# Kernel optimization log

Hardware: AMD Instinct MI355X
Metric: run time of the kernel (lower is better)

Reference implementation:

```python
import jax, jax.numpy as jnp
import numpy as np
from jax import lax

LOG2PI = 1.8378770664093453


def _lstm_last(x, Wih, Whh, b, reverse):
    # x: [N, T, D]; returns hidden output at the LAST timestep index (torch output[:, -1])
    N = x.shape[0]
    H = Whh.shape[1]
    xg = jnp.einsum('ntd,gd->tng', x, Wih) + b  # [T, N, 4H], gate order i,f,g,o

    def step(carry, g_in):
        h, c = carry
        g = g_in + h @ Whh.T
        i, f, gg, o = jnp.split(g, 4, axis=-1)
        c = jax.nn.sigmoid(f) * c + jax.nn.sigmoid(i) * jnp.tanh(gg)
        h = jax.nn.sigmoid(o) * jnp.tanh(c)
        return (h, c), h

    init = (jnp.zeros((N, H), x.dtype), jnp.zeros((N, H), x.dtype))
    _, hs = lax.scan(step, init, xg, reverse=reverse)
    return hs[-1]  # fw: full pass; bw(reverse=True): processed only last element, as torch


def _dvbf(x, u, eps1, eps, fw_Wih, fw_Whh, fw_b, bw_Wih, bw_Whh, bw_b,
          i1_w, i1_b, i2_w, i2_b, z1_w, z1_b, z2_w, z2_b,
          wp_w1, wp_b1, wp_w2, wp_b2, vp_w1, vp_b1, vp_w2, vp_b2,
          ob_w1, ob_b1, ob_w2, ob_b2, A, B, C):
    N, T, dx = x.shape
    dw = eps1.shape[1]
    # initial samples from bidirectional LSTM output at t = T-1 (fw || bw)
    h0 = jnp.concatenate([_lstm_last(x, fw_Wih, fw_Whh, fw_b, False),
                          _lstm_last(x, bw_Wih, bw_Whh, bw_b, True)], axis=1)
    p0 = jax.nn.relu(h0 @ i1_w.T + i1_b) @ i2_w.T + i2_b
    m0, s0_raw = jnp.split(p0, 2, axis=1)
    s0 = jnp.exp(s0_raw) + 1e-5
    w1 = m0 + s0 * eps1  # reparameterized torch.normal(mean, std)
    z1 = jax.nn.relu(w1 @ z1_w.T + z1_b) @ z2_w.T + z2_b

    def step(z_t, inp):
        x_t, u_t, e_t = inp
        pw = jnp.tanh(jnp.concatenate([x_t, z_t, u_t], axis=1) @ wp_w1.T + wp_b1) @ wp_w2.T + wp_b2
        m, s_raw = jnp.split(pw, 2, axis=1)
        s = jnp.exp(s_raw) + 0.01
        w_t = m + s * e_t
        alpha = jax.nn.softmax(
            jax.nn.relu(jnp.concatenate([z_t, u_t], axis=1) @ vp_w1.T + vp_b1) @ vp_w2.T + vp_b2,
            axis=1)
        z_n = (jnp.einsum('nm,mij,nj->ni', alpha, A, z_t)
               + jnp.einsum('nm,mij,nj->ni', alpha, B, u_t)
               + jnp.einsum('nm,mij,nj->ni', alpha, C, w_t))
        return z_n, (z_n, m, s)

    xs = (jnp.swapaxes(x[:, 1:], 0, 1), jnp.swapaxes(u[:, :T - 1], 0, 1), jnp.swapaxes(eps[:, 1:], 0, 1))
    _, (zs, ms, ss) = lax.scan(step, z1, xs)
    z = jnp.concatenate([z1[:, None], jnp.swapaxes(zs, 0, 1)], axis=1)        # [N,T,dz]
    w_mean = jnp.concatenate([m0[:, None], jnp.swapaxes(ms, 0, 1)], axis=1)   # [N,T,dw]
    w_std = jnp.concatenate([s0[:, None], jnp.swapaxes(ss, 0, 1)], axis=1)

    x_rec = jax.nn.relu(z @ ob_w1.T + ob_b1) @ ob_w2.T + ob_b2                # [N,T,dx]
    logprob_x = -0.5 * jnp.sum((x - x_rec) ** 2) - 0.5 * N * T * dx * LOG2PI
    # KL(N(m, diag(std)) || N(0, I)) -- the module uses std as the covariance diagonal
    kl = 0.5 * (jnp.sum(w_std) + jnp.sum(w_mean ** 2) - N * T * dw - jnp.sum(jnp.log(w_std)))
    return -(logprob_x - kl)


def setup_inputs() -> dict:
    key = jax.random.key(0)
    ks = iter(jax.random.split(key, 64))

    def rn(shape, s=1.0):
        return s * jax.random.normal(next(ks), shape, dtype=jnp.float32)

    N, T, DX, DU, DZ, DW, M, H = 512, 128, 256, 32, 128, 64, 16, 128
    S = 0.05  # weight scale keeps the recurrence stable
    return {
        'x': rn((N, T, DX)), 'u': rn((N, T, DU)),
        'eps1': rn((N, DW)), 'eps': rn((N, T, DW)),
        'fw_Wih': rn((4 * H, DX), S), 'fw_Whh': rn((4 * H, H), S), 'fw_b': rn((4 * H,), S),
        'bw_Wih': rn((4 * H, DX), S), 'bw_Whh': rn((4 * H, H), S), 'bw_b': rn((4 * H,), S),
        'i1_w': rn((H, 2 * H), S), 'i1_b': rn((H,), S), 'i2_w': rn((2 * DW, H), S), 'i2_b': rn((2 * DW,), S),
        'z1_w': rn((H, DW), S), 'z1_b': rn((H,), S), 'z2_w': rn((DZ, H), S), 'z2_b': rn((DZ,), S),
        'wp_w1': rn((H, DZ + DU + DX), S), 'wp_b1': rn((H,), S), 'wp_w2': rn((2 * DW, H), S), 'wp_b2': rn((2 * DW,), S),
        'vp_w1': rn((H, DZ + DU), S), 'vp_b1': rn((H,), S), 'vp_w2': rn((M, H), S), 'vp_b2': rn((M,), S),
        'ob_w1': rn((H, DZ), S), 'ob_b1': rn((H,), S), 'ob_w2': rn((DX, H), S), 'ob_b2': rn((DX,), S),
        'A': rn((M, DZ, DZ), S), 'B': rn((M, DZ, DU), S), 'C': rn((M, DZ, DW), S),
    }


def reference(x, u, eps1, eps, fw_Wih, fw_Whh, fw_b, bw_Wih, bw_Whh, bw_b,
              i1_w, i1_b, i2_w, i2_b, z1_w, z1_b, z2_w, z2_b,
              wp_w1, wp_b1, wp_w2, wp_b2, vp_w1, vp_b1, vp_w2, vp_b2,
              ob_w1, ob_b1, ob_w2, ob_b2, A, B, C):
    return _dvbf(x, u, eps1, eps, fw_Wih, fw_Whh, fw_b, bw_Wih, bw_Whh, bw_b,
                 i1_w, i1_b, i2_w, i2_b, z1_w, z1_b, z2_w, z2_b,
                 wp_w1, wp_b1, wp_w2, wp_b2, vp_w1, vp_b1, vp_w2, vp_b2,
                 ob_w1, ob_b1, ob_w2, ob_b2, A, B, C)
```

## Files before the change

### kernel.cpp

```cpp
#include <hip/hip_runtime.h>
#include <stdint.h>
#include <math.h>

#define NB  512
#define TT  128
#define DXX 256
#define DUU 32
#define DZZ 128
#define DWW 64
#define MMM 16
#define HHH 128
#define G4  512

typedef __attribute__((ext_vector_type(8))) short bf16x8;
typedef __attribute__((ext_vector_type(4))) float f32x4;
#define MFMA(a,b,c) __builtin_amdgcn_mfma_f32_16x16x32_bf16(a,b,c,0,0,0)
#define MF8(a,b,c)  __builtin_amdgcn_mfma_f32_16x16x32_fp8_fp8(a,b,c,0,0,0)

__device__ __forceinline__ float sigf(float x){ return 1.f/(1.f+__expf(-x)); }
__device__ __forceinline__ float fast_tanh(float x){
    float e = __expf(2.f*x);
    return 1.f - 2.f/(e + 1.f);
}
__device__ __forceinline__ unsigned int f2bf(float f){
    uint32_t u = __float_as_uint(f);
    uint32_t r = (u + 0x7fffu + ((u >> 16) & 1u)) >> 16;
    return r;
}
__device__ __forceinline__ float bf2f(unsigned short u){
    return __uint_as_float(((uint32_t)u) << 16);
}
__device__ __forceinline__ unsigned int f2e4m3(float f){
    uint32_t u = __float_as_uint(f);
    uint32_t s = (u >> 24) & 0x80u;
    uint32_t a = u & 0x7fffffffu;
    if (a >= 0x43e00000u) return s | 0x7eu;
    int exp = (int)(a >> 23) - 127;
    uint32_t mant = a & 0x7fffffu;
    uint32_t code;
    if (exp >= -6){
        uint32_t keep = ((uint32_t)(exp + 7) << 3) | (mant >> 20);
        uint32_t rem = mant & 0xfffffu;
        if (rem > 0x80000u || (rem == 0x80000u && (keep & 1))) keep++;
        code = keep;
        if (code >= 0x7fu) code = 0x7eu;
    } else {
        int rs = 14 - exp;
        if (rs >= 33) return s;
        uint64_t full = (uint64_t)(mant | 0x800000u);
        uint64_t q = full >> rs;
        uint64_t rem = full & (((uint64_t)1 << rs) - 1);
        uint64_t half = (uint64_t)1 << (rs - 1);
        if (rem > half || (rem == half && (q & 1))) q++;
        code = (uint32_t)q;
    }
    return s | code;
}

__device__ __forceinline__ void stage1k(const void* gsrc, void* ldst, int ln)
{
    __builtin_amdgcn_global_load_lds(
        (const __attribute__((address_space(1))) void*)((const char*)gsrc + ln*16),
        (__attribute__((address_space(3))) void*)ldst, 16, 0, 0);
}
__device__ __forceinline__ void stage32k(const void* gsrc, void* ldst, int tid)
{
    const char* g = (const char*)gsrc;
    char* l = (char*)ldst;
    const int lane = tid & 63;
    const int wv   = tid >> 6;
    #pragma unroll
    for (int it = 0; it < 8; it++){
        const int off = it*4096 + wv*1024;
        __builtin_amdgcn_global_load_lds(
            (const __attribute__((address_space(1))) void*)(g + off + lane*16),
            (__attribute__((address_space(3))) void*)(l + off),
            16, 0, 0);
    }
}

__global__ __launch_bounds__(256) void k_prep8b(
    const float* __restrict__ wp_w1, const float* __restrict__ wp_w2,
    const float* __restrict__ vp_w1, const float* __restrict__ vp_w2,
    const float* __restrict__ Amat,  const float* __restrict__ Bmat,
    const float* __restrict__ Cmat,  unsigned char* __restrict__ frag8)
{
    const int wv = blockIdx.x >> 3, c = blockIdx.x & 7;
    unsigned char* dst = frag8 + (size_t)(wv*8 + c)*8192;
    for (int d = threadIdx.x*4; d < 8192; d += 1024){
        uint32_t pk = 0;
        #pragma unroll
        for (int i = 0; i < 4; i++){
            const int B = d + i;
            const int f = 16*c + (B >> 9), r = B & 511;
            const int lane = r >> 3, jj = r & 7;
            const int col = wv*16 + (lane & 15);
            const int kk = (lane >> 4)*8 + jj;
            float v = 0.f;
            if (f < 4)       v = wp_w1[(size_t)col*416 + 256 + f*32 + kk];
            else if (f < 8)  v = vp_w1[(size_t)col*160 + (f-4)*32 + kk];
            else if (f < 12) v = wp_w2[(size_t)col*128 + (f-8)*32 + kk];
            else if (f < 16){ if (wv == 0) v = vp_w2[(size_t)(col&15)*128 + (f-12)*32 + kk]; }
            else {
                const int fi = f-16, m = fi/7, kt = fi%7;
                const int k = kt*32 + kk;
                if (k < 128)      v = Amat[((size_t)m*128 + col)*128 + k];
                else if (k < 160) v = Bmat[((size_t)m*128 + col)*32 + (k-128)];
                else              v = Cmat[((size_t)m*128 + col)*64 + (k-160)];
            }
            pk |= f2e4m3(v * 16.f) << (8*i);
        }
        *(uint32_t*)(dst + d) = pk;
    }
}

__global__ __launch_bounds__(256) void k_prep_p(
    const float* __restrict__ wp_w1, const float* __restrict__ vp_w1,
    unsigned short* __restrict__ fragP)
{
    const int ct = blockIdx.x / 10, f = blockIdx.x % 10;
    unsigned short* dst = fragP + (size_t)blockIdx.x*512;
    for (int e = threadIdx.x; e < 512; e += 256){
        const int lane = e >> 3, j = e & 7;
        const int col = 16*ct + (lane & 15);
        const int kk = (lane >> 4)*8 + j;
        float v;
        if (f < 8)      v = wp_w1[(size_t)col*416 + f*32 + kk];
        else if (f == 8) v = wp_w1[(size_t)col*416 + 384 + kk];
        else             v = vp_w1[(size_t)col*160 + 128 + kk];
        dst[e] = (unsigned short)f2bf(v);
    }
}

__global__ __launch_bounds__(256) void k_prep_xg(const float* __restrict__ Wih,
                                                 unsigned short* __restrict__ fragx)
{
    const int T = blockIdx.x;
    const int ct = T >> 3, kt = T & 7;
    unsigned short* dst = fragx + (size_t)T*512;
    for (int e = threadIdx.x; e < 512; e += 256){
        const int lane = e >> 3, j = e & 7;
        const int m16 = lane & 15, kq = lane >> 4;
        const int kk = 8*kq + j;
        float v = Wih[(size_t)(16*ct + m16)*DXX + 32*kt + kk];
        dst[e] = (unsigned short)f2bf(v);
    }
}

__global__ __launch_bounds__(256) void k_prep_lo(
    const float* __restrict__ Whh,
    const float* __restrict__ ob_w1, const float* __restrict__ ob_w2,
    unsigned short* __restrict__ blstm, unsigned short* __restrict__ bob)
{
    const int tile = blockIdx.x;
    unsigned short* dst; int lt;
    if (tile < 4){ dst = blstm + (size_t)tile*16384; lt = 1; }
    else { dst = bob + (size_t)(tile-4)*16384; lt = 2; }
    for (int e = threadIdx.x; e < 16384; e += 256){
        const int g = e >> 7, p = e & 127;
        const int s = p >> 3, j = p & 7;
        const int k = ((s ^ (g & 7)) << 3) | j;
        float v;
        if (lt == 1) v = Whh[(size_t)(tile*128 + g)*128 + k];
        else {
            const int tt = tile - 4;
            if (tt == 0) v = ob_w1[g*128 + k];
            else         v = ob_w2[(size_t)((tt-1)*128 + g)*128 + k];
        }
        dst[e] = (unsigned short)f2bf(v);
    }
}

__global__ __launch_bounds__(256) void k_prep_in(
    const float* __restrict__ U, const float* __restrict__ EPS,
    unsigned short* __restrict__ IE, unsigned char* __restrict__ IUf)
{
    const int b  = blockIdx.x;
    const int tt = blockIdx.y;
    const int n0 = b*16;
    unsigned short* de = IE + ((size_t)b*127 + tt)*1024;
    for (int h = threadIdx.x; h < 1024; h += 256){
        const int e2 = h >> 9, l = (h >> 3) & 63, j = h & 7;
        const int r = 8*e2 + (l >> 3);
        de[h] = (unsigned short)f2bf(EPS[((size_t)(n0+r)*TT + tt+1)*DWW + (l&7)*8 + j]);
    }
    unsigned char* df = IUf + ((size_t)b*127 + tt)*512;
    for (int h = threadIdx.x; h < 512; h += 256){
        const int smp = h >> 5, sp = (h >> 3) & 3, j = h & 7;
        const int ud = ((sp ^ (smp & 3))*8) + j;
        df[h] = (unsigned char)f2e4m3(U[((size_t)(n0+smp)*TT + tt)*DUU + ud]);
    }
}

__global__ __launch_bounds__(512) void k_pxu(
    const float* __restrict__ X, const float* __restrict__ U,
    const float* __restrict__ wp_b1, const float* __restrict__ vp_b1,
    const unsigned short* __restrict__ fragP,
    unsigned short* __restrict__ IPx, unsigned short* __restrict__ IPL)
{
    __shared__ __align__(16) short sXl[16*256];
    __shared__ __align__(16) short sUl[16*32];
    const int tid = threadIdx.x;
    const int b = blockIdx.x, t = blockIdx.y;
    const int n0 = b*16;
    const int wv = tid >> 6, ln = tid & 63;
    const int rr = ln & 15, q = ln >> 4;
    const int sx7 = rr & 7;
    {
        const int r = tid >> 5, sl = tid & 31;
        const float* xp = &X[((size_t)(n0+r)*TT + t+1)*DXX + sl*8];
        float4 a0 = *(const float4*)xp;
        float4 a1 = *(const float4*)(xp+4);
        int4 pk;
        pk.x = f2bf(a0.x) | (f2bf(a0.y)<<16);
        pk.y = f2bf(a0.z) | (f2bf(a0.w)<<16);
        pk.z = f2bf(a1.x) | (f2bf(a1.y)<<16);
        pk.w = f2bf(a1.z) | (f2bf(a1.w)<<16);
        *(int4*)&sXl[r*256 + ((sl ^ (r&7))<<3)] = pk;
    }
    {
        const int r = tid >> 5, cc = tid & 31;
        sUl[r*32 + (((cc>>3) ^ (r&3))<<3) + (cc&7)] =
            (unsigned short)f2bf(U[((size_t)(n0+r)*TT + t)*DUU + cc]);
    }
    __syncthreads();
    const short* pA = (const short*)fragP + (size_t)wv*10*512 + ln*8;
    f32x4 d = {0.f,0.f,0.f,0.f};
    #pragma unroll
    for (int kt = 0; kt < 8; kt++){
        bf16x8 a = *(const bf16x8*)(pA + kt*512);
        bf16x8 bx = *(const bf16x8*)&sXl[rr*256 + (((4*kt+q) ^ sx7)<<3)];
        d = MFMA(a, bx, d);
    }
    bf16x8 bu = *(const bf16x8*)&sUl[rr*32 + ((q ^ (rr&3))<<3)];
    d = MFMA(*(const bf16x8*)(pA + 8*512), bu, d);
    f32x4 dl = {0.f,0.f,0.f,0.f};
    dl = MFMA(*(const bf16x8*)(pA + 9*512), bu, dl);
    const f32x4 b1v = *(const f32x4*)&wp_b1[wv*16 + q*4];
    const f32x4 bLv = *(const f32x4*)&vp_b1[wv*16 + q*4];
    d = d + b1v;
    dl = dl + bLv;
    const size_t base = ((size_t)b*127 + t)*2048
                      + rr*128 + (((2*wv + (q>>1)) ^ sx7)<<3) + (q&1)*4;
    uint2 p1, p2;
    p1.x = f2bf(d[0]) | (f2bf(d[1])<<16);
    p1.y = f2bf(d[2]) | (f2bf(d[3])<<16);
    p2.x = f2bf(dl[0]) | (f2bf(dl[1])<<16);
    p2.y = f2bf(dl[2]) | (f2bf(dl[3])<<16);
    *(uint2*)&IPx[base] = p1;
    *(uint2*)&IPL[base] = p2;
}

template<int ACT>
__device__ void dense(const float* __restrict__ W, const float* __restrict__ bias,
                      int C, int K, const float* sIn, int ldi,
                      float* sOut, int ldo, float* sWt)
{
    const int tid = threadIdx.x;
    const int g   = tid & 127;
    const int rq  = tid >> 7;
    const int r0  = 2*rq, r1 = 2*rq+1;
    for (int cb = 0; cb < C; cb += 128){
        float acc0 = 0.f, acc1 = 0.f;
        for (int kb = 0; kb < K; kb += 64){
            const int kw = (K - kb < 64) ? (K - kb) : 64;
            __syncthreads();
            if (kw == 64){
                for (int l = tid; l < 128*64; l += 256){
                    int gg = l >> 6, kk = l & 63;
                    int cx = cb + gg;
                    sWt[gg*65 + kk] = (cx < C) ? W[(size_t)cx*K + kb + kk] : 0.f;
                }
            } else {
                for (int l = tid; l < 128*32; l += 256){
                    int gg = l >> 5, kk = l & 31;
                    int cx = cb + gg;
                    sWt[gg*65 + kk] = (cx < C) ? W[(size_t)cx*K + kb + kk] : 0.f;
                }
            }
            __syncthreads();
            const float* ip0 = sIn + r0*ldi + kb;
            const float* ip1 = sIn + r1*ldi + kb;
            const float* wp  = sWt + g*65;
            #pragma unroll 8
            for (int k = 0; k < kw; k++){
                float wv = wp[k];
                acc0 += ip0[k]*wv;
                acc1 += ip1[k]*wv;
            }
        }
        int cx = cb + g;
        if (cx < C){
            float b = bias ? bias[cx] : 0.f;
            float v0 = acc0 + b, v1 = acc1 + b;
            if (ACT == 1){ v0 = fmaxf(v0, 0.f); v1 = fmaxf(v1, 0.f); }
            else if (ACT == 2){ v0 = fast_tanh(v0); v1 = fast_tanh(v1); }
            sOut[r0*ldo + cx] = v0;
            sOut[r1*ldo + cx] = v1;
        }
    }
}

__global__ __launch_bounds__(512) void k_xg2(const float* __restrict__ X,
                                             const unsigned short* __restrict__ fragx,
                                             const float* __restrict__ bias,
                                             unsigned short* __restrict__ xgb)
{
    __shared__ __align__(16) short sXl[16*256];
    const int tid = threadIdx.x;
    const size_t row0 = (size_t)blockIdx.x * 16;
    const int wv = tid >> 6, ln = tid & 63;
    const int rr = ln & 15, q = ln >> 4;
    const int sx7 = rr & 7;
    {
        const int r = tid >> 5, sl = tid & 31;
        const float* xp = &X[(row0 + r)*DXX + sl*8];
        float4 a0 = *(const float4*)xp;
        float4 a1 = *(const float4*)(xp+4);
        int4 pk;
        pk.x = f2bf(a0.x) | (f2bf(a0.y)<<16);
        pk.y = f2bf(a0.z) | (f2bf(a0.w)<<16);
        pk.z = f2bf(a1.x) | (f2bf(a1.y)<<16);
        pk.w = f2bf(a1.z) | (f2bf(a1.w)<<16);
        *(int4*)&sXl[r*256 + ((sl ^ (r&7))<<3)] = pk;
    }
    __syncthreads();
    #pragma unroll
    for (int ci = 0; ci < 4; ci++){
        const int ct = wv*4 + ci;
        const short* pA = (const short*)fragx + (size_t)(ct*8)*512 + ln*8;
        bf16x8 af[8];
        #pragma unroll
        for (int kt = 0; kt < 8; kt++) af[kt] = *(const bf16x8*)(pA + kt*512);
        f32x4 d = {0.f,0.f,0.f,0.f};
        #pragma unroll
        for (int kt = 0; kt < 8; kt++){
            bf16x8 b = *(const bf16x8*)&sXl[rr*256 + (((4*kt+q) ^ sx7)<<3)];
            d = MFMA(af[kt], b, d);
        }
        const f32x4 bb = *(const f32x4*)&bias[ct*16 + q*4];
        uint2 pk;
        pk.x = f2bf(d[0]+bb[0]) | (f2bf(d[1]+bb[1])<<16);
        pk.y = f2bf(d[2]+bb[2]) | (f2bf(d[3]+bb[3])<<16);
        *(uint2*)&xgb[(row0 + rr)*G4 + ct*16 + q*4] = pk;
    }
}

__global__ __launch_bounds__(256) void k_lstm(const unsigned short* __restrict__ xgb,
                                              const unsigned short* __restrict__ blob,
                                              float* __restrict__ h0)
{
    __shared__ __align__(16) char sWh[4][32768];
    __shared__ __align__(16) float sHh[2][128];
    const int tid = threadIdx.x;
    const int n0 = blockIdx.x * 2;
    const int g = tid & 127, rh = tid >> 7;
    #pragma unroll
    for (int i = 0; i < 4; i++)
        stage32k((const char*)blob + (size_t)i*32768, sWh[i], tid);
    sHh[tid >> 7][tid & 127] = 0.f;
    float cc = 0.f;
    asm volatile("s_waitcnt vmcnt(0)" ::: "memory");
    __syncthreads();
    const size_t xbase = ((size_t)(n0+rh)*TT)*G4 + g;
    for (int t = 0; t < TT; t++){
        float xv[4];
        #pragma unroll
        for (int ct = 0; ct < 4; ct++) xv[ct] = bf2f(xgb[xbase + (size_t)t*G4 + ct*128]);
        float a[4] = {0.f,0.f,0.f,0.f};
        #pragma unroll
        for (int s = 0; s < 16; s++){
            const float* ip = &sHh[rh][s*8];
            float4 u0 = *(const float4*)ip;
            float4 u1 = *(const float4*)(ip+4);
            float in[8] = {u0.x,u0.y,u0.z,u0.w,u1.x,u1.y,u1.z,u1.w};
            #pragma unroll
            for (int ct = 0; ct < 4; ct++){
                const uint32_t* wp = (const uint32_t*)(sWh[ct] + g*256 + ((s ^ (g & 7)) << 4));
                #pragma unroll
                for (int d = 0; d < 4; d++){
                    uint32_t w2 = wp[d];
                    a[ct] = fmaf(__uint_as_float(w2 << 16),        in[2*d],   a[ct]);
                    a[ct] = fmaf(__uint_as_float(w2 & 0xffff0000u), in[2*d+1], a[ct]);
                }
            }
        }
        __syncthreads();
        float ii = sigf(a[0] + xv[0]);
        float ff = sigf(a[1] + xv[1]);
        float gg = fast_tanh(a[2] + xv[2]);
        float oo = sigf(a[3] + xv[3]);
        cc = ff*cc + ii*gg;
        float hh = oo*fast_tanh(cc);
        sHh[rh][g] = hh;
        __syncthreads();
    }
    h0[(size_t)(n0+rh)*HHH + g] = sHh[rh][g];
}

__global__ __launch_bounds__(256) void k_init(
    const float* __restrict__ X,
    const float* __restrict__ bw_Wih, const float* __restrict__ bw_b,
    const float* __restrict__ i1w, const float* __restrict__ i1b,
    const float* __restrict__ i2w, const float* __restrict__ i2b,
    const float* __restrict__ z1w, const float* __restrict__ z1b,
    const float* __restrict__ z2w, const float* __restrict__ z2b,
    const float* __restrict__ eps1, const float* __restrict__ h0,
    float* __restrict__ zb, float* __restrict__ wm, float* __restrict__ wsd)
{
    __shared__ float sX[4*260];
    __shared__ float sG[4*516];
    __shared__ float sH0[4*260];
    __shared__ float sT[4*132];
    __shared__ float sP[4*132];
    __shared__ float sWt[128*65];
    const int tid = threadIdx.x;
    const int n0  = blockIdx.x * 4;
    for (int l = tid; l < 4*256; l += 256){
        int r = l >> 8, k = l & 255;
        sX[r*260+k] = X[((size_t)(n0+r)*TT + (TT-1))*DXX + k];
    }
    for (int l = tid; l < 4*128; l += 256){
        int r = l >> 7, j = l & 127;
        sH0[r*260+j] = h0[(size_t)(n0+r)*HHH + j];
    }
    dense<0>(bw_Wih, bw_b, 512, 256, sX, 260, sG, 516, sWt);
    __syncthreads();
    for (int l = tid; l < 4*128; l += 256){
        int r = l >> 7, j = l & 127;
        float gi = sG[r*516 + j];
        float gv = sG[r*516 + 256 + j];
        float go = sG[r*516 + 384 + j];
        float c  = sigf(gi)*fast_tanh(gv);
        sH0[r*260 + 128 + j] = sigf(go)*fast_tanh(c);
    }
    dense<1>(i1w, i1b, 128, 256, sH0, 260, sT, 132, sWt);
    dense<0>(i2w, i2b, 128, 128, sT, 132, sP, 132, sWt);
    __syncthreads();
    for (int l = tid; l < 4*64; l += 256){
        int r = l >> 6, j = l & 63;
        float m0 = sP[r*132 + j];
        float s0 = __expf(sP[r*132 + 64 + j]) + 1e-5f;
        float w1 = m0 + s0*eps1[(size_t)(n0+r)*DWW + j];
        wm[((size_t)(n0+r)*TT)*DWW + j]  = m0;
        wsd[((size_t)(n0+r)*TT)*DWW + j] = s0;
        sX[r*68 + j] = w1;
    }
    dense<1>(z1w, z1b, 128, 64, sX, 68, sT, 132, sWt);
    dense<0>(z2w, z2b, 128, 128, sT, 132, sP, 132, sWt);
    __syncthreads();
    for (int l = tid; l < 4*128; l += 256){
        int r = l >> 7, j = l & 127;
        zb[((size_t)(n0+r)*TT)*DZZ + j] = sP[r*132+j];
    }
}

#define VWAIT4() do{ asm volatile("s_waitcnt vmcnt(4)" ::: "memory"); \
                    __builtin_amdgcn_sched_barrier(0); }while(0)
#define LWAIT() do{ asm volatile("s_waitcnt lgkmcnt(0)" ::: "memory"); \
                    __builtin_amdgcn_sched_barrier(0); }while(0)
#define BAR()   __builtin_amdgcn_s_barrier()

__global__ __launch_bounds__(512) void k_scan(
    const float* __restrict__ wp_b2, const float* __restrict__ vp_b2,
    const unsigned char* __restrict__ frag8,
    const unsigned short* __restrict__ IPx, const unsigned short* __restrict__ IPL,
    const unsigned short* __restrict__ IE, const unsigned char* __restrict__ IUf,
    float* __restrict__ zb, float* __restrict__ wm, float* __restrict__ wsd)
{
    __shared__ __align__(16) short sRing[32768];
    __shared__ __align__(16) short sHead[32768];
    __shared__ __align__(16) short sPx[2048];
    __shared__ __align__(16) short sPL[2048];
    __shared__ __align__(16) char  sZf[2048];
    __shared__ __align__(16) char  sUf[2][512];
    __shared__ __align__(16) char  sWf[1024];
    __shared__ __align__(16) short sEr[1024];
    __shared__ __align__(16) char  sH1f[2048];
    __shared__ __align__(16) char  sH2f[2048];
    __shared__ __align__(16) float sPW[16*132];
    __shared__ __align__(16) float sL [16*20];
    __shared__ float sAl[16*17];

    const int tid = threadIdx.x;
    const int n0  = blockIdx.x * 16;
    const int wv  = tid >> 6;
    const int ln  = tid & 63;
    const int smp = ln & 15, q = ln >> 4;
    const int sx7 = smp & 7;
    char* ringB = (char*)sRing + wv*8192;
    char* headB = (char*)sHead + wv*8192;
    const unsigned char* myblob = frag8 + (size_t)wv*65536;

    const f32x4 bw2 = *(const f32x4*)&wp_b2[wv*16 + q*4];
    f32x4 bv2 = {0.f,0.f,0.f,0.f};
    if (wv == 0) bv2 = *(const f32x4*)&vp_b2[q*4];

    #define ISSUE_CHUNK(cc_) do{ const int c2_ = (cc_) % 14; \
        _Pragma("unroll") \
        for (int k4 = 0; k4 < 4; k4++) \
            stage1k(myblob + 8192 + (size_t)c2_*4096 + k4*1024, \
                    ringB + (c2_&1)*4096 + k4*1024, ln); }while(0)
    #define HF8(f_)    (*(const long*)(headB + (f_)*512 + ln*8))
    #define AF8(c_,p_) (*(const long*)(ringB + ((c_)&1)*4096 + (p_)*512 + ln*8))
    #define BH1F(t_) (*(const long*)&sH1f[smp*128 + (((4*(t_)+q) ^ sx7)<<3)])
    #define BH2F(t_) (*(const long*)&sH2f[smp*128 + (((4*(t_)+q) ^ sx7)<<3)])

    auto issue_inputs = [&](int tt){
        const size_t ib = (size_t)blockIdx.x*127 + tt;
        if (wv < 4) stage1k((const char*)IPx + ib*4096 + wv*1024, (char*)sPx + wv*1024, ln);
        else        stage1k((const char*)IPL + ib*4096 + (wv-4)*1024, (char*)sPL + (wv-4)*1024, ln);
        if (wv == 0)      stage1k((const char*)IE + ib*2048,        (char*)sEr,        ln);
        else if (wv == 1) stage1k((const char*)IE + ib*2048 + 1024, (char*)sEr + 1024, ln);
        else if (wv == 2){ if (ln < 32) stage1k((const char*)IUf + ib*512, sUf[tt&1], ln); }
    };

    issue_inputs(0);
    if (tid < 256){
        const int zs = tid >> 4, sl = tid & 15;
        const float* zp = &zb[((size_t)(n0+zs)*TT)*DZZ + sl*8];
        float4 a0 = *(const float4*)zp;
        float4 a1 = *(const float4*)(zp+4);
        uint2 p8;
        p8.x = f2e4m3(a0.x) | (f2e4m3(a0.y)<<8) | (f2e4m3(a0.z)<<16) | (f2e4m3(a0.w)<<24);
        p8.y = f2e4m3(a1.x) | (f2e4m3(a1.y)<<8) | (f2e4m3(a1.z)<<16) | (f2e4m3(a1.w)<<24);
        *(uint2*)&sZf[zs*128 + ((sl ^ (zs&7))<<3)] = p8;
    }
    #pragma unroll
    for (int k8 = 0; k8 < 8; k8++)
        stage1k(myblob + k8*1024, headB + k8*1024, ln);
    ISSUE_CHUNK(0);
    ISSUE_CHUNK(1);
    asm volatile("s_waitcnt vmcnt(0)" ::: "memory");
    __builtin_amdgcn_sched_barrier(0);
    LWAIT(); BAR();

    for (int t = 0; t < TT-1; t++){
        long bz0 = *(const long*)&sZf[smp*128 + (((0*4+q) ^ sx7)<<3)];
        long bz1 = *(const long*)&sZf[smp*128 + (((1*4+q) ^ sx7)<<3)];
        long bz2 = *(const long*)&sZf[smp*128 + (((2*4+q) ^ sx7)<<3)];
        long bz3 = *(const long*)&sZf[smp*128 + (((3*4+q) ^ sx7)<<3)];

        f32x4 d1a = {0.f,0.f,0.f,0.f}, d1b = {0.f,0.f,0.f,0.f};
        d1a = MF8(HF8(0), bz0, d1a); d1b = MF8(HF8(1), bz1, d1b);
        d1a = MF8(HF8(2), bz2, d1a); d1b = MF8(HF8(3), bz3, d1b);
        f32x4 d3a = {0.f,0.f,0.f,0.f}, d3b = {0.f,0.f,0.f,0.f};
        d3a = MF8(HF8(4), bz0, d3a); d3b = MF8(HF8(5), bz1, d3b);
        d3a = MF8(HF8(6), bz2, d3a); d3b = MF8(HF8(7), bz3, d3b);
        {
            const int basep = smp*128 + (((2*wv + (q>>1)) ^ sx7)<<3) + (q&1)*4;
            uint2 pxw = *(const uint2*)&sPx[basep];
            uint2 plw = *(const uint2*)&sPL[basep];
            f32x4 d1 = d1a + d1b, d3 = d3a + d3b;
            float v0 = fast_tanh(d1[0]*0.0625f + bf2f((unsigned short)(pxw.x & 0xffff)));
            float v1 = fast_tanh(d1[1]*0.0625f + bf2f((unsigned short)(pxw.x >> 16)));
            float v2 = fast_tanh(d1[2]*0.0625f + bf2f((unsigned short)(pxw.y & 0xffff)));
            float v3 = fast_tanh(d1[3]*0.0625f + bf2f((unsigned short)(pxw.y >> 16)));
            const int baseh = smp*128 + (((2*wv + (q>>1)) ^ sx7)<<3) + (q&1)*4;
            *(unsigned int*)&sH1f[baseh] =
                f2e4m3(v0) | (f2e4m3(v1)<<8) | (f2e4m3(v2)<<16) | (f2e4m3(v3)<<24);
            float w0 = fmaxf(d3[0]*0.0625f + bf2f((unsigned short)(plw.x & 0xffff)), 0.f);
            float w1 = fmaxf(d3[1]*0.0625f + bf2f((unsigned short)(plw.x >> 16)), 0.f);
            float w2 = fmaxf(d3[2]*0.0625f + bf2f((unsigned short)(plw.y & 0xffff)), 0.f);
            float w3 = fmaxf(d3[3]*0.0625f + bf2f((unsigned short)(plw.y >> 16)), 0.f);
            *(unsigned int*)&sH2f[baseh] =
                f2e4m3(w0) | (f2e4m3(w1)<<8) | (f2e4m3(w2)<<16) | (f2e4m3(w3)<<24);
        }
        LWAIT(); BAR();

        {
            f32x4 d2a = {0.f,0.f,0.f,0.f}, d2b = {0.f,0.f,0.f,0.f};
            d2a = MF8(HF8(8),  BH1F(0), d2a); d2b = MF8(HF8(9),  BH1F(1), d2b);
            d2a = MF8(HF8(10), BH1F(2), d2a); d2b = MF8(HF8(11), BH1F(3), d2b);
            f32x4 o = (d2a + d2b)*0.0625f + bw2;
            *(f32x4*)&sPW[smp*132 + wv*16 + q*4] = o;
            if (wv == 0){
                f32x4 d4a = {0.f,0.f,0.f,0.f}, d4b = {0.f,0.f,0.f,0.f};
                d4a = MF8(HF8(12), BH2F(0), d4a); d4b = MF8(HF8(13), BH2F(1), d4b);
                d4a = MF8(HF8(14), BH2F(2), d4a); d4b = MF8(HF8(15), BH2F(3), d4b);
                f32x4 o4 = (d4a + d4b)*0.0625f + bv2;
                *(f32x4*)&sL[smp*20 + q*4] = o4;
            }
        }
        LWAIT(); BAR();

        {
            const int cs = wv, cj = ln;
            float e0 = bf2f((unsigned short)sEr[cs*64 + cj]);
            float e1 = bf2f((unsigned short)sEr[(cs+8)*64 + cj]);
            float m0 = sPW[cs*132 + cj];
            float s0 = __expf(sPW[cs*132 + 64 + cj]) + 0.01f;
            float m1 = sPW[(cs+8)*132 + cj];
            float s1 = __expf(sPW[(cs+8)*132 + 64 + cj]) + 0.01f;
            float w0 = m0 + s0*e0;
            float w1 = m1 + s1*e1;
            wm [((size_t)(n0+cs  )*TT + t+1)*DWW + cj] = m0;
            wsd[((size_t)(n0+cs  )*TT + t+1)*DWW + cj] = s0;
            wm [((size_t)(n0+cs+8)*TT + t+1)*DWW + cj] = m1;
            wsd[((size_t)(n0+cs+8)*TT + t+1)*DWW + cj] = s1;
            const int sw = cj >> 3;
            sWf[ cs   *64 + ((sw ^ ( cs   &7))<<3) + (cj&7)] = (char)f2e4m3(w0);
            sWf[(cs+8)*64 + ((sw ^ ((cs+8)&7))<<3) + (cj&7)] = (char)f2e4m3(w1);
        }
        if (tid < 16){
            float mx = -1e30f;
            #pragma unroll
            for (int m = 0; m < 16; m++) mx = fmaxf(mx, sL[tid*20+m]);
            float ss = 0.f;
            float ex[16];
            #pragma unroll
            for (int m = 0; m < 16; m++){ ex[m] = __expf(sL[tid*20+m]-mx); ss += ex[m]; }
            float inv = 0.0625f/ss;
            #pragma unroll
            for (int m = 0; m < 16; m++) sAl[tid*17+m] = ex[m]*inv;
        }
        if (t < TT-2) issue_inputs(t+1);
        LWAIT(); BAR();

        long bu8 = *(const long*)&sUf[t&1][smp*32 + ((q ^ (smp&3))<<3)];
        long bw80 = *(const long*)&sWf[smp*64 + ((q ^ sx7)<<3)];
        long bw81 = *(const long*)&sWf[smp*64 + (((4+q) ^ sx7)<<3)];
        f32x4 zac = {0.f,0.f,0.f,0.f};
        f32x4 da = {0.f,0.f,0.f,0.f}, db = {0.f,0.f,0.f,0.f};
        #pragma unroll
        for (int c = 0; c < 14; c++){
            VWAIT4();
            #pragma unroll
            for (int p = 0; p < 8; p++){
                const int fi = 8*c + p;
                const int m  = fi/7, kt = fi%7;
                long a = AF8(c, p);
                long b;
                if (kt == 0) b = bz0;
                else if (kt == 1) b = bz1;
                else if (kt == 2) b = bz2;
                else if (kt == 3) b = bz3;
                else if (kt == 4) b = bu8;
                else if (kt == 5) b = bw80;
                else b = bw81;
                if (kt & 1) db = MF8(a, b, db);
                else        da = MF8(a, b, da);
                if (kt == 6){
                    const float al = sAl[smp*17 + m];
                    f32x4 s = da + db;
                    zac[0] += al*s[0]; zac[1] += al*s[1];
                    zac[2] += al*s[2]; zac[3] += al*s[3];
                    da = (f32x4){0.f,0.f,0.f,0.f};
                    db = (f32x4){0.f,0.f,0.f,0.f};
                }
            }
            ISSUE_CHUNK(c+2);
        }
        LWAIT(); BAR();

        {
            const int slotz = 2*wv + (q>>1);
            unsigned int p8 = f2e4m3(zac[0]) | (f2e4m3(zac[1])<<8)
                            | (f2e4m3(zac[2])<<16) | (f2e4m3(zac[3])<<24);
            *(unsigned int*)&sZf[smp*128 + ((slotz ^ sx7)<<3) + (q&1)*4] = p8;
            float4 st = {zac[0], zac[1], zac[2], zac[3]};
            *(float4*)&zb[((size_t)(n0+smp)*TT + t+1)*DZZ + wv*16 + q*4] = st;
        }
        LWAIT(); BAR();
    }
    asm volatile("s_waitcnt vmcnt(0) lgkmcnt(0)" ::: "memory");
    #undef ISSUE_CHUNK
    #undef HF8
    #undef AF8
    #undef BH1F
    #undef BH2F
}

__global__ __launch_bounds__(256) void k_ob(const float* __restrict__ X,
        const float* __restrict__ zb,
        const float* __restrict__ b1, const float* __restrict__ b2,
        const unsigned short* __restrict__ blob, float* __restrict__ acc)
{
    __shared__ __align__(16) char  sW[2][32768];
    __shared__ __align__(16) float sZ[32*128];
    __shared__ __align__(16) float sH[32*128];
    __shared__ float redb[4];
    const int tid = threadIdx.x;
    const size_t row0 = (size_t)blockIdx.x * 32;
    const int g = tid & 127, rh = tid >> 7;
    for (int l = tid; l < 32*128; l += 256)
        sZ[l] = zb[(row0 + (size_t)(l >> 7))*DZZ + (l & 127)];
    stage32k((const char*)blob, sW[0], tid);
    asm volatile("s_waitcnt vmcnt(0)" ::: "memory");
    __syncthreads();
    stage32k((const char*)blob + 32768, sW[1], tid);
    float h[16];
    #pragma unroll
    for (int r = 0; r < 16; r++) h[r] = 0.f;
    #pragma unroll 4
    for (int s = 0; s < 16; s++){
        const uint32_t* wp = (const uint32_t*)(sW[0] + g*256 + ((s ^ (g & 7)) << 4));
        float wv[8];
        #pragma unroll
        for (int d = 0; d < 4; d++){
            uint32_t w2 = wp[d];
            wv[2*d]   = __uint_as_float(w2 << 16);
            wv[2*d+1] = __uint_as_float(w2 & 0xffff0000u);
        }
        #pragma unroll
        for (int r = 0; r < 16; r++){
            const float* ip = &sZ[(rh*16+r)*128 + s*8];
            float4 u0 = *(const float4*)ip;
            float4 u1 = *(const float4*)(ip+4);
            h[r] = fmaf(wv[0],u0.x, fmaf(wv[1],u0.y, fmaf(wv[2],u0.z, fmaf(wv[3],u0.w, h[r]))));
            h[r] = fmaf(wv[4],u1.x, fmaf(wv[5],u1.y, fmaf(wv[6],u1.z, fmaf(wv[7],u1.w, h[r]))));
        }
    }
    {
        const float bb1 = b1[g];
        #pragma unroll
        for (int r = 0; r < 16; r++){
            h[r] = fmaxf(h[r] + bb1, 0.f);
            sH[(rh*16+r)*128 + g] = h[r];
        }
    }
    asm volatile("s_waitcnt vmcnt(0)" ::: "memory");
    __syncthreads();
    float errs = 0.f;
    stage32k((const char*)blob + 65536, sW[0], tid);
    #pragma unroll 1
    for (int cb = 0; cb < 2; cb++){
        const char* wt = cb ? (const char*)sW[0] : (const char*)sW[1];
        float a2[16];
        #pragma unroll
        for (int r = 0; r < 16; r++) a2[r] = 0.f;
        #pragma unroll 4
        for (int s = 0; s < 16; s++){
            const uint32_t* wp = (const uint32_t*)(wt + g*256 + ((s ^ (g & 7)) << 4));
            float wv[8];
            #pragma unroll
            for (int d = 0; d < 4; d++){
                uint32_t w2 = wp[d];
                wv[2*d]   = __uint_as_float(w2 << 16);
                wv[2*d+1] = __uint_as_float(w2 & 0xffff0000u);
            }
            #pragma unroll
            for (int r = 0; r < 16; r++){
                const float* ip = &sH[(rh*16+r)*128 + s*8];
                float4 u0 = *(const float4*)ip;
                float4 u1 = *(const float4*)(ip+4);
                a2[r] = fmaf(wv[0],u0.x, fmaf(wv[1],u0.y, fmaf(wv[2],u0.z, fmaf(wv[3],u0.w, a2[r]))));
                a2[r] = fmaf(wv[4],u1.x, fmaf(wv[5],u1.y, fmaf(wv[6],u1.z, fmaf(wv[7],u1.w, a2[r]))));
            }
        }
        const float bb2 = b2[cb*128 + g];
        #pragma unroll
        for (int r = 0; r < 16; r++){
            float xr = a2[r] + bb2;
            float xv = X[(row0 + rh*16 + r)*DXX + cb*128 + g];
            float e = xv - xr;
            errs += e*e;
        }
        if (cb == 0){
            asm volatile("s_waitcnt vmcnt(0)" ::: "memory");
            __syncthreads();
        }
    }
    for (int o = 32; o > 0; o >>= 1) errs += __shfl_down(errs, o);
    if ((tid & 63) == 0) redb[tid >> 6] = errs;
    __syncthreads();
    if (tid == 0) atomicAdd(acc, redb[0]+redb[1]+redb[2]+redb[3]);
}

__global__ __launch_bounds__(256) void k_kl(const float* __restrict__ wm,
                                            const float* __restrict__ wsd,
                                            float* __restrict__ acc)
{
    __shared__ float red[3][4];
    const int tid = threadIdx.x;
    const size_t base = (size_t)blockIdx.x * 4096 + tid;
    float s2 = 0.f, s3 = 0.f, s4 = 0.f;
    #pragma unroll
    for (int it = 0; it < 16; it++){
        size_t i = base + (size_t)it*256;
        float sd = wsd[i], mv = wm[i];
        s2 += sd; s3 += mv*mv; s4 += __logf(sd);
    }
    for (int o = 32; o > 0; o >>= 1){
        s2 += __shfl_down(s2, o); s3 += __shfl_down(s3, o); s4 += __shfl_down(s4, o);
    }
    if ((tid & 63) == 0){ int w = tid >> 6; red[0][w]=s2; red[1][w]=s3; red[2][w]=s4; }
    __syncthreads();
    if (tid == 0) atomicAdd(acc+1, red[0][0]+red[0][1]+red[0][2]+red[0][3]);
    if (tid == 1) atomicAdd(acc+2, red[1][0]+red[1][1]+red[1][2]+red[1][3]);
    if (tid == 2) atomicAdd(acc+3, red[2][0]+red[2][1]+red[2][2]+red[2][3]);
}

__global__ void k_final(const float* __restrict__ acc, float* __restrict__ out)
{
    if (threadIdx.x == 0 && blockIdx.x == 0){
        const double LOG2PI = 1.8378770664093453;
        double logpx_c = 0.5 * (double)NB * TT * DXX * LOG2PI;
        double kl = 0.5 * ((double)acc[1] + (double)acc[2]
                           - (double)NB*TT*DWW - (double)acc[3]);
        out[0] = (float)(0.5*(double)acc[0] + logpx_c + kl);
    }
}

extern "C" void kernel_launch(void* const* d_in, const int* in_sizes, int n_in,
                              void* d_out, int out_size, void* d_ws, size_t ws_size,
                              hipStream_t stream)
{
    (void)in_sizes; (void)n_in; (void)out_size; (void)ws_size;
    const float* x      = (const float*)d_in[0];
    const float* u      = (const float*)d_in[1];
    const float* eps1   = (const float*)d_in[2];
    const float* eps    = (const float*)d_in[3];
    const float* fw_Wih = (const float*)d_in[4];
    const float* fw_Whh = (const float*)d_in[5];
    const float* fw_b   = (const float*)d_in[6];
    const float* bw_Wih = (const float*)d_in[7];
    const float* bw_b   = (const float*)d_in[9];
    const float* i1w = (const float*)d_in[10];
    const float* i1b = (const float*)d_in[11];
    const float* i2w = (const float*)d_in[12];
    const float* i2b = (const float*)d_in[13];
    const float* z1w = (const float*)d_in[14];
    const float* z1b = (const float*)d_in[15];
    const float* z2w = (const float*)d_in[16];
    const float* z2b = (const float*)d_in[17];
    const float* wp_w1 = (const float*)d_in[18];
    const float* wp_b1 = (const float*)d_in[19];
    const float* wp_w2 = (const float*)d_in[20];
    const float* wp_b2 = (const float*)d_in[21];
    const float* vp_w1 = (const float*)d_in[22];
    const float* vp_b1 = (const float*)d_in[23];
    const float* vp_w2 = (const float*)d_in[24];
    const float* vp_b2 = (const float*)d_in[25];
    const float* ob_w1 = (const float*)d_in[26];
    const float* ob_b1 = (const float*)d_in[27];
    const float* ob_w2 = (const float*)d_in[28];
    const float* ob_b2 = (const float*)d_in[29];
    const float* Amat  = (const float*)d_in[30];
    const float* Bmat  = (const float*)d_in[31];
    const float* Cmat  = (const float*)d_in[32];
    float* out = (float*)d_out;

    unsigned short* xgb = (unsigned short*)d_ws;
    float* h0  = (float*)(xgb + (size_t)NB*TT*G4);
    float* zb  = h0  + (size_t)NB*HHH;
    float* wm  = zb  + (size_t)NB*TT*DZZ;
    float* wsd = wm  + (size_t)NB*TT*DWW;
    float* acc = wsd + (size_t)NB*TT*DWW;
    unsigned short* blstm = (unsigned short*)(acc + 64);
    unsigned short* bob   = blstm + (size_t)4*16384;
    unsigned short* bfragx= bob   + (size_t)3*16384;
    unsigned short* fragP = bfragx+ (size_t)256*512;
    unsigned char*  frag8 = (unsigned char*)(fragP + (size_t)80*512);
    unsigned short* IPx   = (unsigned short*)(frag8 + (size_t)8*65536);
    unsigned short* IPL   = IPx + (size_t)32*127*2048;
    unsigned short* IE    = IPL + (size_t)32*127*2048;
    unsigned char*  IUf   = (unsigned char*)(IE + (size_t)32*127*1024);

    hipMemsetAsync(acc, 0, 4*sizeof(float), stream);

    k_prep8b<<<64, 256, 0, stream>>>(wp_w1, wp_w2, vp_w1, vp_w2,
                                     Amat, Bmat, Cmat, frag8);
    k_prep_p<<<80, 256, 0, stream>>>(wp_w1, vp_w1, fragP);
    k_prep_xg<<<256, 256, 0, stream>>>(fw_Wih, bfragx);
    k_prep_lo<<<7, 256, 0, stream>>>(fw_Whh, ob_w1, ob_w2, blstm, bob);
    k_prep_in<<<dim3(32,127), 256, 0, stream>>>(u, eps, IE, IUf);
    k_pxu <<<dim3(32,127), 512, 0, stream>>>(x, u, wp_b1, vp_b1, fragP, IPx, IPL);
    k_xg2 <<<NB*TT/16, 512, 0, stream>>>(x, bfragx, fw_b, xgb);
    k_lstm<<<NB/2, 256, 0, stream>>>(xgb, blstm, h0);
    k_init<<<NB/4, 256, 0, stream>>>(x, bw_Wih, bw_b, i1w, i1b, i2w, i2b,
                                     z1w, z1b, z2w, z2b, eps1, h0, zb, wm, wsd);
    k_scan<<<32, 512, 0, stream>>>(wp_b2, vp_b2, frag8, IPx, IPL, IE, IUf,
                                   zb, wm, wsd);
    k_ob  <<<NB*TT/32, 256, 0, stream>>>(x, zb, ob_b1, ob_b2, bob, acc);
    k_kl  <<<NB*TT*DWW/4096, 256, 0, stream>>>(wm, wsd, acc);
    k_final<<<1, 64, 0, stream>>>(acc, out);
}
```

Before: 2.686 ms.

## Stream transition-matrix fp8 fragments from global into registers, drop LDS ring

The scan kernel's per-step mixture weights (A/B/C as fp8 MFMA fragments) are now loaded with vector global loads straight into registers, double-buffered across chunks. This replaces the LDS ring that was filled by global_load_lds. The prep kernel re-lays out the fragments so each lane reads 64 contiguous bytes per chunk. The aim is to cut LDS write/read traffic and free 64KB of shared memory. In exchange it adds register pressure and exposes L2 latency, with only the vmcnt waits hiding it.

```diff
diff --git a/kernel.cpp b/kernel.cpp
--- a/kernel.cpp
+++ b/kernel.cpp
@@ -14,6 +14,7 @@
 
 typedef __attribute__((ext_vector_type(8))) short bf16x8;
 typedef __attribute__((ext_vector_type(4))) float f32x4;
+typedef __attribute__((ext_vector_type(2))) long longx2;
 #define MFMA(a,b,c) __builtin_amdgcn_mfma_f32_16x16x32_bf16(a,b,c,0,0,0)
 #define MF8(a,b,c)  __builtin_amdgcn_mfma_f32_16x16x32_fp8_fp8(a,b,c,0,0,0)
 
@@ -85,25 +86,31 @@
     const float* __restrict__ Amat,  const float* __restrict__ Bmat,
     const float* __restrict__ Cmat,  unsigned char* __restrict__ frag8)
 {
-    const int wv = blockIdx.x >> 3, c = blockIdx.x & 7;
-    unsigned char* dst = frag8 + (size_t)(wv*8 + c)*8192;
+    const int wv = blockIdx.x >> 3, cc = blockIdx.x & 7;
+    unsigned char* dst = frag8 + (size_t)wv*65536 + (size_t)cc*8192;
     for (int d = threadIdx.x*4; d < 8192; d += 1024){
         uint32_t pk = 0;
         #pragma unroll
         for (int i = 0; i < 4; i++){
             const int B = d + i;
-            const int f = 16*c + (B >> 9), r = B & 511;
-            const int lane = r >> 3, jj = r & 7;
-            const int col = wv*16 + (lane & 15);
-            const int kk = (lane >> 4)*8 + jj;
             float v = 0.f;
-            if (f < 4)       v = wp_w1[(size_t)col*416 + 256 + f*32 + kk];
-            else if (f < 8)  v = vp_w1[(size_t)col*160 + (f-4)*32 + kk];
-            else if (f < 12) v = wp_w2[(size_t)col*128 + (f-8)*32 + kk];
-            else if (f < 16){ if (wv == 0) v = vp_w2[(size_t)(col&15)*128 + (f-12)*32 + kk]; }
-            else {
-                const int fi = f-16, m = fi/7, kt = fi%7;
-                const int k = kt*32 + kk;
+            if (cc == 0){
+                const int f = B >> 9, r = B & 511;
+                const int lane = r >> 3, jj = r & 7;
+                const int col = wv*16 + (lane & 15);
+                const int kk = (lane >> 4)*8 + jj;
+                if (f < 4)       v = wp_w1[(size_t)col*416 + 256 + f*32 + kk];
+                else if (f < 8)  v = vp_w1[(size_t)col*160 + (f-4)*32 + kk];
+                else if (f < 12) v = wp_w2[(size_t)col*128 + (f-8)*32 + kk];
+                else { if (wv == 0) v = vp_w2[(size_t)(col&15)*128 + (f-12)*32 + kk]; }
+            } else {
+                const int c = 2*(cc-1) + (B >> 12);
+                const int r = B & 4095;
+                const int lane = r >> 6, f8 = (r >> 3) & 7, b = r & 7;
+                const int fi = 8*c + f8;
+                const int m = fi/7, kt = fi%7;
+                const int col = wv*16 + (lane & 15);
+                const int k = kt*32 + (lane >> 4)*8 + b;
                 if (k < 128)      v = Amat[((size_t)m*128 + col)*128 + k];
                 else if (k < 160) v = Bmat[((size_t)m*128 + col)*32 + (k-128)];
                 else              v = Cmat[((size_t)m*128 + col)*64 + (k-160)];
@@ -455,7 +462,7 @@
     }
 }
 
-#define VWAIT4() do{ asm volatile("s_waitcnt vmcnt(4)" ::: "memory"); \
+#define VWAITR() do{ asm volatile("s_waitcnt vmcnt(4)" ::: "memory"); \
                     __builtin_amdgcn_sched_barrier(0); }while(0)
 #define LWAIT() do{ asm volatile("s_waitcnt lgkmcnt(0)" ::: "memory"); \
                     __builtin_amdgcn_sched_barrier(0); }while(0)
@@ -468,7 +475,6 @@
     const unsigned short* __restrict__ IE, const unsigned char* __restrict__ IUf,
     float* __restrict__ zb, float* __restrict__ wm, float* __restrict__ wsd)
 {
-    __shared__ __align__(16) short sRing[32768];
     __shared__ __align__(16) short sHead[32768];
     __shared__ __align__(16) short sPx[2048];
     __shared__ __align__(16) short sPL[2048];
@@ -488,21 +494,18 @@
     const int ln  = tid & 63;
     const int smp = ln & 15, q = ln >> 4;
     const int sx7 = smp & 7;
-    char* ringB = (char*)sRing + wv*8192;
     char* headB = (char*)sHead + wv*8192;
     const unsigned char* myblob = frag8 + (size_t)wv*65536;
+    const char* abase = (const char*)myblob + 8192 + ln*64;
 
     const f32x4 bw2 = *(const f32x4*)&wp_b2[wv*16 + q*4];
     f32x4 bv2 = {0.f,0.f,0.f,0.f};
     if (wv == 0) bv2 = *(const f32x4*)&vp_b2[q*4];
 
-    #define ISSUE_CHUNK(cc_) do{ const int c2_ = (cc_) % 14; \
-        _Pragma("unroll") \
-        for (int k4 = 0; k4 < 4; k4++) \
-            stage1k(myblob + 8192 + (size_t)c2_*4096 + k4*1024, \
-                    ringB + (c2_&1)*4096 + k4*1024, ln); }while(0)
+    #define LOADC(r0_,r1_,r2_,r3_,c_) do{ const char* gp_ = abase + (size_t)(c_)*4096; \
+        r0_ = *(const longx2*)(gp_);      r1_ = *(const longx2*)(gp_+16); \
+        r2_ = *(const longx2*)(gp_+32);   r3_ = *(const longx2*)(gp_+48); }while(0)
     #define HF8(f_)    (*(const long*)(headB + (f_)*512 + ln*8))
-    #define AF8(c_,p_) (*(const long*)(ringB + ((c_)&1)*4096 + (p_)*512 + ln*8))
     #define BH1F(t_) (*(const long*)&sH1f[smp*128 + (((4*(t_)+q) ^ sx7)<<3)])
     #define BH2F(t_) (*(const long*)&sH2f[smp*128 + (((4*(t_)+q) ^ sx7)<<3)])
 
@@ -529,11 +532,13 @@
     #pragma unroll
     for (int k8 = 0; k8 < 8; k8++)
         stage1k(myblob + k8*1024, headB + k8*1024, ln);
-    ISSUE_CHUNK(0);
-    ISSUE_CHUNK(1);
     asm volatile("s_waitcnt vmcnt(0)" ::: "memory");
     __builtin_amdgcn_sched_barrier(0);
     LWAIT(); BAR();
+
+    longx2 rA0, rA1, rA2, rA3, rB0, rB1, rB2, rB3;
+    LOADC(rA0,rA1,rA2,rA3, 0);
+    LOADC(rB0,rB1,rB2,rB3, 1);
 
     for (int t = 0; t < TT-1; t++){
         long bz0 = *(const long*)&sZf[smp*128 + (((0*4+q) ^ sx7)<<3)];
@@ -556,14 +561,13 @@
             float v1 = fast_tanh(d1[1]*0.0625f + bf2f((unsigned short)(pxw.x >> 16)));
             float v2 = fast_tanh(d1[2]*0.0625f + bf2f((unsigned short)(pxw.y & 0xffff)));
             float v3 = fast_tanh(d1[3]*0.0625f + bf2f((unsigned short)(pxw.y >> 16)));
-            const int baseh = smp*128 + (((2*wv + (q>>1)) ^ sx7)<<3) + (q&1)*4;
-            *(unsigned int*)&sH1f[baseh] =
+            *(unsigned int*)&sH1f[basep] =
                 f2e4m3(v0) | (f2e4m3(v1)<<8) | (f2e4m3(v2)<<16) | (f2e4m3(v3)<<24);
             float w0 = fmaxf(d3[0]*0.0625f + bf2f((unsigned short)(plw.x & 0xffff)), 0.f);
             float w1 = fmaxf(d3[1]*0.0625f + bf2f((unsigned short)(plw.x >> 16)), 0.f);
             float w2 = fmaxf(d3[2]*0.0625f + bf2f((unsigned short)(plw.y & 0xffff)), 0.f);
             float w3 = fmaxf(d3[3]*0.0625f + bf2f((unsigned short)(plw.y >> 16)), 0.f);
-            *(unsigned int*)&sH2f[baseh] =
+            *(unsigned int*)&sH2f[basep] =
                 f2e4m3(w0) | (f2e4m3(w1)<<8) | (f2e4m3(w2)<<16) | (f2e4m3(w3)<<24);
         }
         LWAIT(); BAR();
@@ -622,35 +626,37 @@
         long bw81 = *(const long*)&sWf[smp*64 + (((4+q) ^ sx7)<<3)];
         f32x4 zac = {0.f,0.f,0.f,0.f};
         f32x4 da = {0.f,0.f,0.f,0.f}, db = {0.f,0.f,0.f,0.f};
-        #pragma unroll
-        for (int c = 0; c < 14; c++){
-            VWAIT4();
-            #pragma unroll
-            for (int p = 0; p < 8; p++){
-                const int fi = 8*c + p;
-                const int m  = fi/7, kt = fi%7;
-                long a = AF8(c, p);
-                long b;
-                if (kt == 0) b = bz0;
-                else if (kt == 1) b = bz1;
-                else if (kt == 2) b = bz2;
-                else if (kt == 3) b = bz3;
-                else if (kt == 4) b = bu8;
-                else if (kt == 5) b = bw80;
-                else b = bw81;
-                if (kt & 1) db = MF8(a, b, db);
-                else        da = MF8(a, b, da);
-                if (kt == 6){
-                    const float al = sAl[smp*17 + m];
-                    f32x4 s = da + db;
-                    zac[0] += al*s[0]; zac[1] += al*s[1];
-                    zac[2] += al*s[2]; zac[3] += al*s[3];
-                    da = (f32x4){0.f,0.f,0.f,0.f};
-                    db = (f32x4){0.f,0.f,0.f,0.f};
-                }
-            }
-            ISSUE_CHUNK(c+2);
-        }
+        #define CHUNK_MFMA(R0_,R1_,R2_,R3_,c_) do{ \
+            _Pragma("unroll") \
+            for (int p = 0; p < 8; p++){ \
+                const int fi = 8*(c_) + p; \
+                const int m_ = fi/7, kt_ = fi%7; \
+                long a_ = (p<2) ? R0_[p&1] : (p<4) ? R1_[p&1] : (p<6) ? R2_[p&1] : R3_[p&1]; \
+                long b_; \
+                if (kt_ == 0) b_ = bz0; else if (kt_ == 1) b_ = bz1; \
+                else if (kt_ == 2) b_ = bz2; else if (kt_ == 3) b_ = bz3; \
+                else if (kt_ == 4) b_ = bu8; else if (kt_ == 5) b_ = bw80; \
+                else b_ = bw81; \
+                if (kt_ & 1) db = MF8(a_, b_, db); else da = MF8(a_, b_, da); \
+                if (kt_ == 6){ \
+                    const float al_ = sAl[smp*17 + m_]; \
+                    f32x4 s_ = da + db; \
+                    zac[0] += al_*s_[0]; zac[1] += al_*s_[1]; \
+                    zac[2] += al_*s_[2]; zac[3] += al_*s_[3]; \
+                    da = (f32x4){0.f,0.f,0.f,0.f}; \
+                    db = (f32x4){0.f,0.f,0.f,0.f}; \
+                } \
+            } }while(0)
+        #pragma unroll
+        for (int cp = 0; cp < 7; cp++){
+            VWAITR();
+            CHUNK_MFMA(rA0,rA1,rA2,rA3, 2*cp);
+            LOADC(rA0,rA1,rA2,rA3, (2*cp+2) % 14);
+            VWAITR();
+            CHUNK_MFMA(rB0,rB1,rB2,rB3, 2*cp+1);
+            LOADC(rB0,rB1,rB2,rB3, (2*cp+3) % 14);
+        }
+        #undef CHUNK_MFMA
         LWAIT(); BAR();
 
         {
@@ -664,9 +670,8 @@
         LWAIT(); BAR();
     }
     asm volatile("s_waitcnt vmcnt(0) lgkmcnt(0)" ::: "memory");
-    #undef ISSUE_CHUNK
+    #undef LOADC
     #undef HF8
-    #undef AF8
     #undef BH1F
     #undef BH2F
 }
```

Result: faster. 2.578 ms (-4.0%).
